# Optimization experiments

Hardware: AMD Instinct MI355X
Metric: run time of the kernel (lower is better)

## Reference

```python
import jax, jax.numpy as jnp
import numpy as np

L = 65536      # number of received symbols
MT = 64        # Mtestangles
NF = 64        # averaging half-window -> filter length 2*NF+1 = 129


def setup_inputs() -> dict:
    key = jax.random.key(0)
    k1, k2 = jax.random.split(key, 2)
    # 64-QAM constellation, unit average power
    pts = jnp.arange(-7, 8, 2, dtype=jnp.float32)  # 8 PAM levels
    re, im = jnp.meshgrid(pts, pts, indexing='ij')
    sym = (re + 1j * im).reshape(-1)
    sym = sym / jnp.sqrt(jnp.mean(jnp.abs(sym) ** 2))
    # received signal: random constellation symbols + slow phase drift + noise
    idx = jax.random.randint(k1, (L,), 0, sym.shape[0])
    drift = jnp.cumsum(0.002 * jax.random.normal(k2, (L,), jnp.float32))
    noise = 0.05 * (jax.random.normal(jax.random.fold_in(key, 7), (L,), jnp.float32)
                    + 1j * jax.random.normal(jax.random.fold_in(key, 8), (L,), jnp.float32))
    x = sym[idx] * jnp.exp(1j * drift) + noise
    # triangular averaging filter: [1..N+1, N..1]
    avg_filter = jnp.concatenate([
        jnp.arange(1, NF + 2, dtype=jnp.float32),
        jnp.arange(NF, 0, -1, dtype=jnp.float32)])
    return {
        'x_real': x.real.astype(jnp.float32),
        'x_imag': x.imag.astype(jnp.float32),
        'symbols_real': sym.real.astype(jnp.float32),
        'symbols_imag': sym.imag.astype(jnp.float32),
        'avg_filter': avg_filter,
        'temperature': jnp.array([0.05], dtype=jnp.float32),
    }


def reference(x_real, x_imag, symbols_real, symbols_imag, avg_filter, temperature):
    # angles for no_sectors==4: linspace(-pi/4, pi/4 - (pi/2)/M, M)
    angles = jnp.linspace(-np.pi / 4, np.pi / 4 - (np.pi / 2) / MT, MT).astype(jnp.float32)  # [M]
    x = jax.lax.complex(x_real, x_imag)                       # [L]
    EE = x[:, None] * jnp.exp(1j * angles)                    # [L, M] rotated copies
    # dist[l,m] = min_s |EE - s|^2 = |x|^2 + min_s(|s|^2 - 2 Re(EE conj(s)))
    sym_sq = symbols_real ** 2 + symbols_imag ** 2            # [S]
    cross = EE.real[:, :, None] * symbols_real + EE.imag[:, :, None] * symbols_imag  # [L, M, S]
    dist = (x_real ** 2 + x_imag ** 2)[:, None] + jnp.min(sym_sq - 2.0 * cross, axis=2)  # [L, M]
    # sliding-window average along time (torch conv1d padding='same', normalized taps)
    w = avg_filter / jnp.sum(avg_filter)                      # [2N+1]
    mvg = jax.lax.conv_general_dilated(
        dist.T[:, None, :],            # [M, 1, L]
        w[None, None, :],              # [1, 1, 2N+1]
        window_strides=(1,), padding=[(NF, NF)],
        dimension_numbers=('NCH', 'OIH', 'NCH'))[:, 0, :].T   # [L, M]
    mvg = mvg / jnp.sum(mvg, axis=1, keepdims=True)
    # softmin over test angles
    smvg = jax.nn.softmax(-mvg / temperature[0], axis=1)      # [L, M]
    sang = 4.0 * angles
    ang = jnp.arctan2(smvg @ jnp.sin(sang), smvg @ jnp.cos(sang))  # [L]
    ph = jnp.unwrap(ang, discont=np.pi, period=2 * np.pi) / 4.0
    out = x * jnp.exp(1j * ph)
    return out, ph
```

## Files before the change

kernel.cpp:

```cpp
#include <hip/hip_runtime.h>


#define LN   65536
#define PI_F 3.14159265358979323846f
#define TWO_PI_F 6.2831853071795864769f

#define CORR(dd) (((dd) < -PI_F) ? 1 : (((dd) > PI_F) ? -1 : 0))

__global__ __launch_bounds__(256) void v11_stage_ang(const float* __restrict__ xr,
                                                     const float* __restrict__ xi,
                                                     const float* __restrict__ temp,
                                                     float* __restrict__ ang_out) {
    __shared__ float P1[64 * 193];
    __shared__ float xsr[192], xsi[192];
    __shared__ float tot1[4][64];
    __shared__ float tot2[4][64];
    __shared__ float s4v[64], c4v[64];

    const int t   = threadIdx.x;
    const int l0  = blockIdx.x * 64;
    const int m   = t & 63;
    const int seg = t >> 6;

    if (t < 192) {
        int gl = l0 - 64 + t;
        bool ok = (unsigned)gl < (unsigned)LN;
        xsr[t] = ok ? xr[gl] : 0.0f;
        xsi[t] = ok ? xi[gl] : 0.0f;
    }
    if (t < 64) {
        float a4 = (float)t * (PI_F / 32.0f) - PI_F;
        float s, c; sincosf(a4, &s, &c);
        s4v[t] = s; c4v[t] = c;
    }
    __syncthreads();

    {
        const float am = (float)m * (PI_F / 128.0f) - (PI_F * 0.25f);
        float sm, cm; sincosf(am, &sm, &cm);
        const float SQ = 6.4807406984078602f;
        const float cq = cm * SQ, sq = sm * SQ;
        float pr[48];
        float p = 0.0f;
        #pragma unroll
        for (int i = 0; i < 48; ++i) {
            int li = seg * 48 + i;
            float a = xsr[li], b = xsi[li];
            float tr = a * cq - b * sq;
            float ti = a * sq + b * cq;
            float rr = fminf(fmaxf(rintf(fmaf(tr, 0.5f, 3.5f)), 0.0f), 7.0f);
            float ri = fminf(fmaxf(rintf(fmaf(ti, 0.5f, 3.5f)), 0.0f), 7.0f);
            float dr = fmaf(-2.0f, rr, tr + 7.0f);
            float di = fmaf(-2.0f, ri, ti + 7.0f);
            float d = fmaf(dr, dr, di * di) * (1.0f / 42.0f);
            d = ((unsigned)(l0 - 64 + li) < (unsigned)LN) ? d : 0.0f;
            p += d;
            pr[i] = p;
        }
        tot1[seg][m] = p;
        __syncthreads();
        float off = 0.0f;
        #pragma unroll
        for (int s = 0; s < 3; ++s) if (s < seg) off += tot1[s][m];
        #pragma unroll
        for (int i = 0; i < 48; ++i) P1[m * 193 + seg * 48 + i] = pr[i] + off;
    }
    __syncthreads();

    const int jn = (seg < 3) ? 33 : 30;
    const int j0 = seg * 33;
    {
        float q[33];
        float p2 = 0.0f;
        #pragma unroll
        for (int i = 0; i < 33; ++i) {
            if (i < jn) {
                int j = j0 + i;
                float hi = P1[m * 193 + 63 + j];
                float lo = (j >= 2) ? P1[m * 193 + j - 2] : 0.0f;
                p2 += hi - lo;
                q[i] = p2;
            }
        }
        tot2[seg][m] = p2;
        __syncthreads();
        float off2 = 0.0f;
        #pragma unroll
        for (int s = 0; s < 3; ++s) if (s < seg) off2 += tot2[s][m];
        float* Q = P1;
        #pragma unroll
        for (int i = 0; i < 33; ++i) if (i < jn) Q[m * 131 + j0 + i] = q[i] + off2;
    }
    __syncthreads();

    {
        const float* Q = P1;
        const float T = temp[0];
        const int lane = t & 63;
        const int sub  = lane & 3;
        const int r    = (t >> 6) * 16 + (lane >> 2);
        const int mb   = sub * 16;

        float v[16];
        float rs = 0.0f, mn = 3.4e38f;
        #pragma unroll
        for (int i = 0; i < 16; ++i) {
            int mm = mb + i;
            float vv = Q[mm * 131 + r + 65] - Q[mm * 131 + r];
            v[i] = vv; rs += vv; mn = fminf(mn, vv);
        }
        rs += __shfl_xor(rs, 1, 64); rs += __shfl_xor(rs, 2, 64);
        mn = fminf(mn, __shfl_xor(mn, 1, 64)); mn = fminf(mn, __shfl_xor(mn, 2, 64));

        float inv = 1.0f / (rs * T);
        float ss = 0.0f, sc = 0.0f;
        #pragma unroll
        for (int i = 0; i < 16; ++i) {
            int mm = mb + i;
            float e = __expf((mn - v[i]) * inv);
            ss = fmaf(e, s4v[mm], ss);
            sc = fmaf(e, c4v[mm], sc);
        }
        ss += __shfl_xor(ss, 1, 64); ss += __shfl_xor(ss, 2, 64);
        sc += __shfl_xor(sc, 1, 64); sc += __shfl_xor(sc, 2, 64);
        if (sub == 0) ang_out[l0 + r] = atan2f(ss, sc);
    }
}

__global__ __launch_bounds__(256) void v11_scan_local(const float* __restrict__ ang,
                                                      int* __restrict__ klocal,
                                                      int* __restrict__ bsum) {
    __shared__ int wtot[4];
    const int t = threadIdx.x;
    const int b = blockIdx.x;
    const int e = b * 256 + t;
    const int i4 = e * 4;

    float4 a = *(const float4*)(ang + i4);
    float prev = (i4 == 0) ? 0.0f : ang[i4 - 1];

    int s0 = CORR(a.x - prev);
    int s1 = CORR(a.y - a.x);
    int s2 = CORR(a.z - a.y);
    int s3 = CORR(a.w - a.z);
    int k0 = s0, k1 = k0 + s1, k2 = k1 + s2, k3 = k2 + s3;

    const int lane = t & 63, wv = t >> 6;
    int scan = k3;
    #pragma unroll
    for (int off = 1; off < 64; off <<= 1) {
        int v = __shfl_up(scan, off, 64);
        if (lane >= off) scan += v;
    }
    if (lane == 63) wtot[wv] = scan;
    __syncthreads();
    int woff = 0;
    #pragma unroll
    for (int j = 0; j < 3; ++j) if (j < wv) woff += wtot[j];
    const int excl = woff + scan - k3;

    ((int4*)klocal)[e] = make_int4(excl + k0, excl + k1, excl + k2, excl + k3);
    if (t == 255) bsum[b] = woff + scan;
}

__global__ __launch_bounds__(512) void v11_stage_out(const float* __restrict__ xr,
                                                     const float* __restrict__ xi,
                                                     const float* __restrict__ ang,
                                                     const int* __restrict__ klocal,
                                                     const int* __restrict__ bsum,
                                                     float* __restrict__ out_base) {
    __shared__ int s_boff;
    const int t = threadIdx.x;
    const int b = blockIdx.x;
    const int chunk = b >> 1;

    if (t < 64) {
        int v = (t < chunk) ? bsum[t] : 0;
        #pragma unroll
        for (int off = 1; off < 64; off <<= 1) v += __shfl_xor(v, off, 64);
        if (t == 0) s_boff = v;
    }
    __syncthreads();

    const int l = b * 512 + t;
    float ph = (ang[l] + TWO_PI_F * (float)(klocal[l] + s_boff)) * 0.25f;
    float s, c; sincosf(ph, &s, &c);
    float a = xr[l], bb = xi[l];
    out_base[l]      = a * c - bb * s;
    out_base[LN + l] = ph;
}

extern "C" void kernel_launch(void* const* d_in, const int* in_sizes, int n_in,
                              void* d_out, int out_size, void* d_ws, size_t ws_size,
                              hipStream_t stream) {
    (void)in_sizes; (void)n_in; (void)out_size; (void)ws_size;
    const float* xr   = (const float*)d_in[0];
    const float* xi   = (const float*)d_in[1];
    const float* temp = (const float*)d_in[5];

    float* ang    = (float*)d_ws;
    int*   klocal = (int*)((char*)d_ws + LN * sizeof(float));
    int*   bsum   = (int*)((char*)d_ws + 2 * LN * sizeof(float));

    v11_stage_ang <<<LN / 64, 256, 0, stream>>>(xr, xi, temp, ang);
    v11_scan_local<<<64, 256, 0, stream>>>(ang, klocal, bsum);
    v11_stage_out <<<LN / 512, 512, 0, stream>>>(xr, xi, ang, klocal, bsum, (float*)d_out);
}
```

Measured before the change: 77.65 us.

## Fuse unwrap scan and output stage using a single-pass lookback

After: 79.69 us. 2.6% more time.

```diff
diff --git a/kernel.cpp b/kernel.cpp
--- a/kernel.cpp
+++ b/kernel.cpp
@@ -7,12 +7,12 @@
 
 #define CORR(dd) (((dd) < -PI_F) ? 1 : (((dd) > PI_F) ? -1 : 0))
 
-__global__ __launch_bounds__(256) void v11_stage_ang(const float* __restrict__ xr,
+__global__ __launch_bounds__(256) void v13_stage_ang(const float* __restrict__ xr,
                                                      const float* __restrict__ xi,
                                                      const float* __restrict__ temp,
                                                      float* __restrict__ ang_out) {
-    __shared__ float P1[64 * 193];
-    __shared__ float xsr[192], xsi[192];
+    __shared__ __align__(16) float P1[64 * 193];
+    __shared__ __align__(16) float2 xs2[192];
     __shared__ float tot1[4][64];
     __shared__ float tot2[4][64];
     __shared__ float s4v[64], c4v[64];
@@ -25,8 +25,7 @@
     if (t < 192) {
         int gl = l0 - 64 + t;
         bool ok = (unsigned)gl < (unsigned)LN;
-        xsr[t] = ok ? xr[gl] : 0.0f;
-        xsi[t] = ok ? xi[gl] : 0.0f;
+        xs2[t] = make_float2(ok ? xr[gl] : 0.0f, ok ? xi[gl] : 0.0f);
     }
     if (t < 64) {
         float a4 = (float)t * (PI_F / 32.0f) - PI_F;
@@ -43,19 +42,31 @@
         float pr[48];
         float p = 0.0f;
         #pragma unroll
-        for (int i = 0; i < 48; ++i) {
+        for (int i = 0; i < 48; i += 2) {
             int li = seg * 48 + i;
-            float a = xsr[li], b = xsi[li];
-            float tr = a * cq - b * sq;
-            float ti = a * sq + b * cq;
-            float rr = fminf(fmaxf(rintf(fmaf(tr, 0.5f, 3.5f)), 0.0f), 7.0f);
-            float ri = fminf(fmaxf(rintf(fmaf(ti, 0.5f, 3.5f)), 0.0f), 7.0f);
-            float dr = fmaf(-2.0f, rr, tr + 7.0f);
-            float di = fmaf(-2.0f, ri, ti + 7.0f);
-            float d = fmaf(dr, dr, di * di) * (1.0f / 42.0f);
-            d = ((unsigned)(l0 - 64 + li) < (unsigned)LN) ? d : 0.0f;
-            p += d;
-            pr[i] = p;
+            float4 xx = *(const float4*)(&xs2[li]);
+            {
+                float tr = xx.x * cq - xx.y * sq;
+                float ti = xx.x * sq + xx.y * cq;
+                float rr = fminf(fmaxf(rintf(fmaf(tr, 0.5f, 3.5f)), 0.0f), 7.0f);
+                float ri = fminf(fmaxf(rintf(fmaf(ti, 0.5f, 3.5f)), 0.0f), 7.0f);
+                float dr = fmaf(-2.0f, rr, tr + 7.0f);
+                float di = fmaf(-2.0f, ri, ti + 7.0f);
+                float d = fmaf(dr, dr, di * di) * (1.0f / 42.0f);
+                d = ((unsigned)(l0 - 64 + li) < (unsigned)LN) ? d : 0.0f;
+                p += d; pr[i] = p;
+            }
+            {
+                float tr = xx.z * cq - xx.w * sq;
+                float ti = xx.z * sq + xx.w * cq;
+                float rr = fminf(fmaxf(rintf(fmaf(tr, 0.5f, 3.5f)), 0.0f), 7.0f);
+                float ri = fminf(fmaxf(rintf(fmaf(ti, 0.5f, 3.5f)), 0.0f), 7.0f);
+                float dr = fmaf(-2.0f, rr, tr + 7.0f);
+                float di = fmaf(-2.0f, ri, ti + 7.0f);
+                float d = fmaf(dr, dr, di * di) * (1.0f / 42.0f);
+                d = ((unsigned)(l0 - 64 + li + 1) < (unsigned)LN) ? d : 0.0f;
+                p += d; pr[i + 1] = p;
+            }
         }
         tot1[seg][m] = p;
         __syncthreads();
@@ -127,10 +138,14 @@
     }
 }
 
-__global__ __launch_bounds__(256) void v11_scan_local(const float* __restrict__ ang,
-                                                      int* __restrict__ klocal,
-                                                      int* __restrict__ bsum) {
+__global__ __launch_bounds__(256) void v13_scan_out(const float* __restrict__ xr,
+                                                    const float* __restrict__ xi,
+                                                    const float* __restrict__ ang,
+                                                    int* __restrict__ partial,
+                                                    int* __restrict__ flags,
+                                                    float* __restrict__ out_base) {
     __shared__ int wtot[4];
+    __shared__ int s_boff;
     const int t = threadIdx.x;
     const int b = blockIdx.x;
     const int e = b * 256 + t;
@@ -159,35 +174,37 @@
     for (int j = 0; j < 3; ++j) if (j < wv) woff += wtot[j];
     const int excl = woff + scan - k3;
 
-    ((int4*)klocal)[e] = make_int4(excl + k0, excl + k1, excl + k2, excl + k3);
-    if (t == 255) bsum[b] = woff + scan;
-}
-
-__global__ __launch_bounds__(512) void v11_stage_out(const float* __restrict__ xr,
-                                                     const float* __restrict__ xi,
-                                                     const float* __restrict__ ang,
-                                                     const int* __restrict__ klocal,
-                                                     const int* __restrict__ bsum,
-                                                     float* __restrict__ out_base) {
-    __shared__ int s_boff;
-    const int t = threadIdx.x;
-    const int b = blockIdx.x;
-    const int chunk = b >> 1;
-
+    if (t == 0) {
+        int btot = wtot[0] + wtot[1] + wtot[2] + wtot[3];
+        __hip_atomic_store(&partial[b], btot, __ATOMIC_RELAXED, __HIP_MEMORY_SCOPE_AGENT);
+        __hip_atomic_store(&flags[b], 1, __ATOMIC_RELEASE, __HIP_MEMORY_SCOPE_AGENT);
+    }
     if (t < 64) {
-        int v = (t < chunk) ? bsum[t] : 0;
+        int v = 0;
+        if (t < b) {
+            while (__hip_atomic_load(&flags[t], __ATOMIC_ACQUIRE, __HIP_MEMORY_SCOPE_AGENT) != 1) {}
+            v = __hip_atomic_load(&partial[t], __ATOMIC_RELAXED, __HIP_MEMORY_SCOPE_AGENT);
+        }
         #pragma unroll
         for (int off = 1; off < 64; off <<= 1) v += __shfl_xor(v, off, 64);
         if (t == 0) s_boff = v;
     }
     __syncthreads();
-
-    const int l = b * 512 + t;
-    float ph = (ang[l] + TWO_PI_F * (float)(klocal[l] + s_boff)) * 0.25f;
-    float s, c; sincosf(ph, &s, &c);
-    float a = xr[l], bb = xi[l];
-    out_base[l]      = a * c - bb * s;
-    out_base[LN + l] = ph;
+    const int boff = s_boff;
+
+    float4 xa = *(const float4*)(xr + i4);
+    float4 xb = *(const float4*)(xi + i4);
+    float ph0 = (a.x + TWO_PI_F * (float)(boff + excl + k0)) * 0.25f;
+    float ph1 = (a.y + TWO_PI_F * (float)(boff + excl + k1)) * 0.25f;
+    float ph2 = (a.z + TWO_PI_F * (float)(boff + excl + k2)) * 0.25f;
+    float ph3 = (a.w + TWO_PI_F * (float)(boff + excl + k3)) * 0.25f;
+    float s0f, c0f, s1f, c1f, s2f, c2f, s3f, c3f;
+    sincosf(ph0, &s0f, &c0f); sincosf(ph1, &s1f, &c1f);
+    sincosf(ph2, &s2f, &c2f); sincosf(ph3, &s3f, &c3f);
+    float4 re = make_float4(xa.x * c0f - xb.x * s0f, xa.y * c1f - xb.y * s1f,
+                            xa.z * c2f - xb.z * s2f, xa.w * c3f - xb.w * s3f);
+    *(float4*)(out_base + i4)      = re;
+    *(float4*)(out_base + LN + i4) = make_float4(ph0, ph1, ph2, ph3);
 }
 
 extern "C" void kernel_launch(void* const* d_in, const int* in_sizes, int n_in,
@@ -198,11 +215,10 @@
     const float* xi   = (const float*)d_in[1];
     const float* temp = (const float*)d_in[5];
 
-    float* ang    = (float*)d_ws;
-    int*   klocal = (int*)((char*)d_ws + LN * sizeof(float));
-    int*   bsum   = (int*)((char*)d_ws + 2 * LN * sizeof(float));
-
-    v11_stage_ang <<<LN / 64, 256, 0, stream>>>(xr, xi, temp, ang);
-    v11_scan_local<<<64, 256, 0, stream>>>(ang, klocal, bsum);
-    v11_stage_out <<<LN / 512, 512, 0, stream>>>(xr, xi, ang, klocal, bsum, (float*)d_out);
+    float* ang     = (float*)d_ws;
+    int*   partial = (int*)((char*)d_ws + LN * sizeof(float));
+    int*   flags   = (int*)((char*)d_ws + LN * sizeof(float) + 256);
+
+    v13_stage_ang<<<LN / 64, 256, 0, stream>>>(xr, xi, temp, ang);
+    v13_scan_out <<<64, 256, 0, stream>>>(xr, xi, ang, partial, flags, (float*)d_out);
 }
```
